# Performance work log

Hardware: AMD Instinct MI355X
Metric: run time of the kernel (lower is better)

Reference implementation:

```python
import jax, jax.numpy as jnp
import numpy as np

B, N, D, H = 2048, 100, 512, 8
TANH_C = 10.0


def setup_inputs() -> dict:
    key = jax.random.key(0)
    ks = jax.random.split(key, 16)
    s = 1.0 / np.sqrt(D)
    inp = {
        "node_embeddings": jax.random.normal(ks[0], (B, N, D), jnp.float32),
        "graph_embedding": jax.random.normal(ks[1], (B, D), jnp.float32),
        "target_idx": jax.random.randint(ks[2], (B,), 0, N, jnp.int32),
        "mask": jax.random.randint(ks[3], (B, N), 0, 2, jnp.int32),
    }
    for i, name in enumerate(["W_target", "W_global", "W_K1", "W_K2", "W_Q", "W_V",
                              "Wq_mha", "Wk_mha", "Wv_mha", "Wo_mha"]):
        inp[name] = jax.random.normal(ks[4 + i], (D, D), jnp.float32) * s
    return inp


def reference(node_embeddings, graph_embedding, target_idx, mask,
              W_target, W_global, W_K1, W_K2, W_Q, W_V,
              Wq_mha, Wk_mha, Wv_mha, Wo_mha):
    # one pointer-network decode step (Decoder loop body)
    b, n, d = node_embeddings.shape
    dh = d // H
    scale_h = 1.0 / (dh ** 0.5)

    # target_embeddings = node_embeddings[arange(B), env.target_stack]
    tgt = jnp.take_along_axis(node_embeddings, target_idx[:, None, None].astype(jnp.int32), axis=1)[:, 0, :]  # [B,D]

    # context = W_target(tgt) + W_global(graph)   (nn.Linear: x @ W.T)
    context = (tgt @ W_target.T + graph_embedding @ W_global.T)[:, None, :]  # [B,1,D]
    node_keys = node_embeddings @ W_K1.T   # [B,N,D]
    node_vals = node_embeddings @ W_V.T    # [B,N,D]

    # MultiHeadAttention([context, keys, values]) with internal per-head projections
    q = (context @ Wq_mha.T).reshape(b, 1, H, dh)
    k = (node_keys @ Wk_mha.T).reshape(b, n, H, dh)
    v = (node_vals @ Wv_mha.T).reshape(b, n, H, dh)
    scores = jnp.einsum("bqhd,bnhd->bhqn", q, k) * scale_h   # [B,H,1,N]
    attn = jax.nn.softmax(scores, axis=-1)
    mha = jnp.einsum("bhqn,bnhd->bqhd", attn, v).reshape(b, 1, d) @ Wo_mha.T  # [B,1,D]

    query = mha @ W_Q.T                    # [B,1,D]
    key2 = node_embeddings @ W_K2.T        # [B,N,D]

    # logits = (query @ key2^T) / sqrt(D), tanh-clipped, masked
    logits = jnp.einsum("bqd,bnd->bqn", query, key2)[:, 0, :] / (d ** 0.5)  # [B,N]
    logits = TANH_C * jnp.tanh(logits)
    logits = logits - mask.astype(logits.dtype) * 1e9
    log_p = jax.nn.log_softmax(logits, axis=1)  # [B,N]
    return log_p
```

## Files before the change

### kernel.cpp

```cpp
#include <hip/hip_runtime.h>

#define DD 512
#define NNODE 100
#define NH 8

typedef __attribute__((ext_vector_type(4))) float f32x4;
typedef __attribute__((ext_vector_type(8))) short s16x8;

__device__ __forceinline__ unsigned short f2bf(float x) {
  union { float f; unsigned int u; } v; v.f = x;
  unsigned int r = v.u + 0x7fffu + ((v.u >> 16) & 1u);
  return (unsigned short)(r >> 16);
}
__device__ __forceinline__ float bf2f(unsigned short u) {
  union { unsigned int u; float f; } v; v.u = ((unsigned int)u) << 16;
  return v.f;
}

__device__ __forceinline__ void gemm_accum(
    f32x4 acc[2][2], const float* __restrict__ A, const float* __restrict__ B,
    const int* __restrict__ gidx, int gmul, int K, int lda, int ldb,
    int transB, int m0, int n0,
    unsigned short (*As)[40], unsigned short (*Bs)[40])
{
  const int t = threadIdx.x;
  const int wid = t >> 6, lane = t & 63;
  const int wr = wid >> 1, wc = wid & 1;
  const int r16 = lane & 15, kg = (lane >> 4) * 8;
  const int tr = t >> 3, kq = t & 7;
  const int bn = t & 63, bk = t >> 6;

  for (int k0 = 0; k0 < K; k0 += 32) {
#pragma unroll
    for (int rp = 0; rp < 2; ++rp) {
      const int row = tr + rp * 32;
      const int gi = m0 + row;
      long ab = (long)gi * lda;
      if (gidx) ab += (long)gidx[gi] * gmul;
      const float4 av = *(const float4*)(A + ab + k0 + kq * 4);
      unsigned int p0 = (unsigned)f2bf(av.x) | ((unsigned)f2bf(av.y) << 16);
      unsigned int p1 = (unsigned)f2bf(av.z) | ((unsigned)f2bf(av.w) << 16);
      *(uint2*)(&As[row][kq * 4]) = make_uint2(p0, p1);
    }
    if (transB) {
#pragma unroll
      for (int rp = 0; rp < 2; ++rp) {
        const int row = tr + rp * 32;
        const float4 bv = *(const float4*)(B + (long)(n0 + row) * ldb + k0 + kq * 4);
        unsigned int p0 = (unsigned)f2bf(bv.x) | ((unsigned)f2bf(bv.y) << 16);
        unsigned int p1 = (unsigned)f2bf(bv.z) | ((unsigned)f2bf(bv.w) << 16);
        *(uint2*)(&Bs[row][kq * 4]) = make_uint2(p0, p1);
      }
    } else {
#pragma unroll
      for (int pp = 0; pp < 8; ++pp) {
        const int k = bk + pp * 4;
        Bs[bn][k] = f2bf(B[(long)(k0 + k) * ldb + n0 + bn]);
      }
    }
    __syncthreads();
    s16x8 a0 = *(const s16x8*)(&As[wr * 32 + r16][kg]);
    s16x8 a1 = *(const s16x8*)(&As[wr * 32 + 16 + r16][kg]);
    s16x8 b0 = *(const s16x8*)(&Bs[wc * 32 + r16][kg]);
    s16x8 b1 = *(const s16x8*)(&Bs[wc * 32 + 16 + r16][kg]);
    acc[0][0] = __builtin_amdgcn_mfma_f32_16x16x32_bf16(a0, b0, acc[0][0], 0, 0, 0);
    acc[0][1] = __builtin_amdgcn_mfma_f32_16x16x32_bf16(a0, b1, acc[0][1], 0, 0, 0);
    acc[1][0] = __builtin_amdgcn_mfma_f32_16x16x32_bf16(a1, b0, acc[1][0], 0, 0, 0);
    acc[1][1] = __builtin_amdgcn_mfma_f32_16x16x32_bf16(a1, b1, acc[1][1], 0, 0, 0);
    __syncthreads();
  }
}

__device__ __forceinline__ void gemm_epilogue(
    f32x4 acc[2][2], void* Cv, int ldc, float alpha, float beta, int obf16,
    int m0, int n0)
{
  const int t = threadIdx.x;
  const int wid = t >> 6, lane = t & 63;
  const int wr = wid >> 1, wc = wid & 1;
  const int r16 = lane & 15;
#pragma unroll
  for (int si = 0; si < 2; ++si)
#pragma unroll
    for (int sj = 0; sj < 2; ++sj)
#pragma unroll
      for (int r = 0; r < 4; ++r) {
        const int row = m0 + wr * 32 + si * 16 + (lane >> 4) * 4 + r;
        const int col = n0 + wc * 32 + sj * 16 + r16;
        const long ci = (long)row * ldc + col;
        float v = alpha * acc[si][sj][r];
        if (obf16) {
          ((unsigned short*)Cv)[ci] = f2bf(v);
        } else {
          float* C = (float*)Cv;
          if (beta != 0.f) v = fmaf(beta, C[ci], v);
          C[ci] = v;
        }
      }
}

__global__ __launch_bounds__(256) void gemm_mfma(
    const float* __restrict__ A, const float* __restrict__ B, void* Cv,
    int K, int lda, int ldb, int ldc,
    long aoffz, long boffz, long coffz,
    int transB, float alpha, float beta, int obf16)
{
  __shared__ unsigned short As[64][40];
  __shared__ unsigned short Bs[64][40];
  A += (long)blockIdx.z * aoffz;
  B += (long)blockIdx.z * boffz;
  f32x4 acc[2][2] = {};
  gemm_accum(acc, A, B, nullptr, 0, K, lda, ldb, transB,
             blockIdx.y * 64, blockIdx.x * 64, As, Bs);
  void* Cz = obf16 ? (void*)((unsigned short*)Cv + (long)blockIdx.z * coffz)
                   : (void*)((float*)Cv + (long)blockIdx.z * coffz);
  gemm_epilogue(acc, Cz, ldc, alpha, beta, obf16, blockIdx.y * 64, blockIdx.x * 64);
}

struct Fold5Args {
  const float* A[5]; const float* B[5]; float* C[5]; float al[5];
};

__global__ __launch_bounds__(256) void fold5_kernel(Fold5Args fa) {
  __shared__ unsigned short As[64][40];
  __shared__ unsigned short Bs[64][40];
  const int z = blockIdx.z;
  f32x4 acc[2][2] = {};
  gemm_accum(acc, fa.A[z], fa.B[z], nullptr, 0, 512, 512, 512, 0,
             blockIdx.y * 64, blockIdx.x * 64, As, Bs);
  gemm_epilogue(acc, fa.C[z], 512, fa.al[z], 0.f, 0, blockIdx.y * 64, blockIdx.x * 64);
}

__global__ __launch_bounds__(256) void qbuf_kernel(
    const float* __restrict__ node, const float* __restrict__ graph,
    const int* __restrict__ tidx, const float* __restrict__ A1,
    const float* __restrict__ A2, float* __restrict__ C)
{
  __shared__ unsigned short As[64][40];
  __shared__ unsigned short Bs[64][40];
  f32x4 acc[2][2] = {};
  gemm_accum(acc, node, A1, tidx, DD, DD, NNODE * DD, DD, 1,
             blockIdx.y * 64, blockIdx.x * 64, As, Bs);
  __syncthreads();
  gemm_accum(acc, graph, A2, nullptr, 0, DD, DD, DD, 1,
             blockIdx.y * 64, blockIdx.x * 64, As, Bs);
  gemm_epilogue(acc, C, DD, 1.f, 0.f, 0, blockIdx.y * 64, blockIdx.x * 64);
}

__global__ __launch_bounds__(256) void attn_fused(
    const float* __restrict__ node, const unsigned short* __restrict__ qk16,
    unsigned short* __restrict__ nb16, float* __restrict__ ctx)
{
  const int b = blockIdx.x;
  const int t = threadIdx.x;
  const int lane = t & 63;
  const int wid = t >> 6;
  const int r16 = lane & 15;
  const int rg = lane >> 4;

  __shared__ unsigned short nf[2][16 * 512];
  __shared__ unsigned short qf[16 * 288];
  __shared__ float Pl[4][16][8];
  __shared__ float rfl[4][8];

  {
    const unsigned short* qb = qk16 + (long)b * (NH * DD);
    for (int slot = t; slot < 512; slot += 256) {
      const int s = slot >> 5;
      const int idx = slot & 31;
      const int h = idx >> 2, g = idx & 3;
      *(s16x8*)(&qf[s * 288 + idx * 8 + (idx >> 3) * 8]) =
          *(const s16x8*)(qb + h * DD + s * 32 + g * 8);
    }
  }

  const int r0 = t >> 7;
  const int c4 = (t * 4) & 511;
  const int slotbase = ((c4 >> 3) * 16) + r0;
  const int j_c = c4 & 7;
  const int d0 = t * 2;
  const int cslot0 = (d0 >> 3) * 16;
  const int cxor = (d0 >> 3) & 7;
  const int cj = d0 & 7;
  const int qidx = (r16 & 7) * 4 + rg;
  const int qfb = qidx * 8 + (qidx >> 3) * 8;

  const float* nbase = node + (long)b * (NNODE * DD);
  float4 rs[8];
  {
    const int lim = NNODE * DD;
#pragma unroll
    for (int i = 0; i < 8; ++i) {
      const int e = 4 * t + 1024 * i;
      rs[i] = (e < lim) ? *(const float4*)(nbase + e) : make_float4(0.f, 0.f, 0.f, 0.f);
    }
  }

  float m = -3.0e38f, l = 0.f;
  float2 c2[NH];
#pragma unroll
  for (int h = 0; h < NH; ++h) { c2[h].x = 0.f; c2[h].y = 0.f; }
  ushort4 h4s[8];

  for (int c = 0; c < 7; ++c) {
    const int c0 = c * 16;
    const int cur = c & 1;
#pragma unroll
    for (int i = 0; i < 8; ++i) {
      ushort4 h4;
      h4.x = f2bf(rs[i].x); h4.y = f2bf(rs[i].y);
      h4.z = f2bf(rs[i].z); h4.w = f2bf(rs[i].w);
      h4s[i] = h4;
      const int slot = slotbase + 2 * i;
      const int phys = slot ^ ((slot >> 4) & 7);
      *(ushort4*)(&nf[cur][phys * 8 + j_c]) = h4;
    }
    __syncthreads();
    if (c < 6) {
      const int nc0 = c0 + 16;
      const int lim = (NNODE - nc0) * DD;
#pragma unroll
      for (int i = 0; i < 8; ++i) {
        const int e = 4 * t + 1024 * i;
        rs[i] = (e < lim) ? *(const float4*)(nbase + (long)nc0 * DD + e)
                          : make_float4(0.f, 0.f, 0.f, 0.f);
      }
    }
#pragma unroll
    for (int i = 0; i < 8; ++i) {
      const int row = r0 + 2 * i;
      if (c0 + row < NNODE)
        *(ushort4*)(nb16 + ((long)b * NNODE + c0 + row) * DD + c4) = h4s[i];
    }

    f32x4 acc = {0.f, 0.f, 0.f, 0.f};
#pragma unroll
    for (int s = 0; s < 16; ++s) {
      const int slr = (s * 4 + rg) * 16 + r16;
      const s16x8 av = *(const s16x8*)(&nf[cur][(slr ^ ((s * 4 + rg) & 7)) * 8]);
      s16x8 bv = {0, 0, 0, 0, 0, 0, 0, 0};
      if (r16 < NH) bv = *(const s16x8*)(&qf[s * 288 + qfb]);
      acc = __builtin_amdgcn_mfma_f32_16x16x32_bf16(av, bv, acc, 0, 0, 0);
    }
#pragma unroll
    for (int r = 0; r < 4; ++r)
      if (c0 + rg * 4 + r >= NNODE) acc[r] = -3.0e38f;

    float cm = fmaxf(fmaxf(acc[0], acc[1]), fmaxf(acc[2], acc[3]));
    cm = fmaxf(cm, __shfl_xor(cm, 16));
    cm = fmaxf(cm, __shfl_xor(cm, 32));
    const float mn = fmaxf(m, cm);
    const float rf = __expf(m - mn);
    float p[4], ps = 0.f;
#pragma unroll
    for (int r = 0; r < 4; ++r) { p[r] = __expf(acc[r] - mn); ps += p[r]; }
    ps += __shfl_xor(ps, 16);
    ps += __shfl_xor(ps, 32);
    l = l * rf + ps;
    m = mn;
    if (r16 < NH) {
#pragma unroll
      for (int r = 0; r < 4; ++r) Pl[wid][rg * 4 + r][r16] = p[r];
      if (rg == 0) rfl[wid][r16] = rf;
    }
    asm volatile("s_waitcnt lgkmcnt(0)" ::: "memory");

    {
      const f32x4 rf0 = *(const f32x4*)(&rfl[wid][0]);
      const f32x4 rf1 = *(const f32x4*)(&rfl[wid][4]);
#pragma unroll
      for (int h = 0; h < 4; ++h) { c2[h].x *= rf0[h]; c2[h].y *= rf0[h]; }
#pragma unroll
      for (int h = 0; h < 4; ++h) { c2[4 + h].x *= rf1[h]; c2[4 + h].y *= rf1[h]; }
#pragma unroll
      for (int n = 0; n < 16; ++n) {
        const int cphys = (cslot0 + n) ^ cxor;
        const unsigned int nv = *(const unsigned int*)(&nf[cur][cphys * 8 + cj]);
        const float x0 = bf2f((unsigned short)(nv & 0xffffu));
        const float x1 = bf2f((unsigned short)(nv >> 16));
        const f32x4 p0 = *(const f32x4*)(&Pl[wid][n][0]);
        const f32x4 p1 = *(const f32x4*)(&Pl[wid][n][4]);
#pragma unroll
        for (int h = 0; h < 4; ++h) {
          c2[h].x = fmaf(p0[h], x0, c2[h].x);
          c2[h].y = fmaf(p0[h], x1, c2[h].y);
          c2[4 + h].x = fmaf(p1[h], x0, c2[4 + h].x);
          c2[4 + h].y = fmaf(p1[h], x1, c2[4 + h].y);
        }
      }
    }
  }

  if (r16 < NH && rg == 0) rfl[wid][r16] = 1.f / l;
  asm volatile("s_waitcnt lgkmcnt(0)" ::: "memory");
  {
    const f32x4 i0 = *(const f32x4*)(&rfl[wid][0]);
    const f32x4 i1 = *(const f32x4*)(&rfl[wid][4]);
    float* cb = ctx + (long)b * (NH * DD) + d0;
#pragma unroll
    for (int h = 0; h < 4; ++h) {
      cb[h * DD] = c2[h].x * i0[h];
      cb[h * DD + 1] = c2[h].y * i0[h];
      cb[(4 + h) * DD] = c2[4 + h].x * i1[h];
      cb[(4 + h) * DD + 1] = c2[4 + h].y * i1[h];
    }
  }
}

__global__ __launch_bounds__(256) void logits_kernel(
    const unsigned short* __restrict__ nb16, const unsigned short* __restrict__ qk216,
    const int* __restrict__ mask, float* __restrict__ out)
{
  const int b = blockIdx.x;
  const int t = threadIdx.x;
  const int wid = t >> 6, lane = t & 63;
  const int r16 = lane & 15, rg = lane >> 4;
  __shared__ float sl[112];
  const unsigned short* qb = qk216 + (long)b * DD + rg * 8;

  for (int ti = wid; ti < 7; ti += 4) {
    const int arow = min(ti * 16 + r16, NNODE - 1);
    const unsigned short* ap = nb16 + ((long)b * NNODE + arow) * DD + rg * 8;
    f32x4 acc = {0.f, 0.f, 0.f, 0.f};
#pragma unroll
    for (int s = 0; s < 16; ++s) {
      const s16x8 av = *(const s16x8*)(ap + s * 32);
      const s16x8 bv = *(const s16x8*)(qb + s * 32);
      acc = __builtin_amdgcn_mfma_f32_16x16x32_bf16(av, bv, acc, 0, 0, 0);
    }
    if (r16 == 0) {
#pragma unroll
      for (int r = 0; r < 4; ++r) {
        const int n = ti * 16 + rg * 4 + r;
        if (n < 112) sl[n] = acc[r];
      }
    }
  }
  __syncthreads();
  if (t < 64) {
    float v0 = -3.0e38f, v1 = -3.0e38f;
    if (lane < NNODE)
      v0 = 10.f * tanhf(sl[lane]) - (float)mask[b * NNODE + lane] * 1e9f;
    if (lane + 64 < NNODE)
      v1 = 10.f * tanhf(sl[lane + 64]) - (float)mask[b * NNODE + lane + 64] * 1e9f;
    float mx = fmaxf(v0, v1);
#pragma unroll
    for (int off = 1; off < 64; off <<= 1) mx = fmaxf(mx, __shfl_xor(mx, off));
    float e = 0.f;
    if (lane < NNODE) e += __expf(v0 - mx);
    if (lane + 64 < NNODE) e += __expf(v1 - mx);
#pragma unroll
    for (int off = 1; off < 64; off <<= 1) e += __shfl_xor(e, off);
    const float lse = mx + __logf(e);
    float* ob = out + (long)b * NNODE;
    if (lane < NNODE) ob[lane] = v0 - lse;
    if (lane + 64 < NNODE) ob[lane + 64] = v1 - lse;
  }
}

extern "C" void kernel_launch(void* const* d_in, const int* in_sizes, int n_in,
                              void* d_out, int out_size, void* d_ws, size_t ws_size,
                              hipStream_t stream) {
  const float* node     = (const float*)d_in[0];
  const float* graph    = (const float*)d_in[1];
  const int*   tidx     = (const int*)d_in[2];
  const int*   mask     = (const int*)d_in[3];
  const float* W_target = (const float*)d_in[4];
  const float* W_global = (const float*)d_in[5];
  const float* W_K1     = (const float*)d_in[6];
  const float* W_K2     = (const float*)d_in[7];
  const float* W_Q      = (const float*)d_in[8];
  const float* W_V      = (const float*)d_in[9];
  const float* Wq_mha   = (const float*)d_in[10];
  const float* Wk_mha   = (const float*)d_in[11];
  const float* Wv_mha   = (const float*)d_in[12];
  const float* Wo_mha   = (const float*)d_in[13];
  float* out = (float*)d_out;

  float* base = (float*)d_ws;
  unsigned short* nb16 = (unsigned short*)base;
  long off = 2048L * NNODE * DD / 2;
  float* A1 = base + off;        off += 262144;
  float* A2 = base + off;        off += 262144;
  float* Wkc = base + off;       off += 262144;
  float* Wvc = base + off;       off += 262144;
  float* Woq = base + off;       off += 262144;
  float* qbuf = base + off;      off += 2048L * 512;
  unsigned short* qk16 = (unsigned short*)(base + off);  off += 2048L * 4096 / 2;
  float* ctxb = base + off;      off += 2048L * 4096;
  float* preo = base + off;      off += 2048L * 512;
  float* query = base + off;     off += 2048L * 512;
  unsigned short* qk216 = (unsigned short*)(base + off); off += 2048L * 512 / 2;

  dim3 blk(256);
  const float SH = 0.125f;
  const float SD = 0.044194173824f;

  Fold5Args fa;
  fa.A[0] = Wq_mha;  fa.B[0] = W_target; fa.C[0] = A1;  fa.al[0] = 1.f;
  fa.A[1] = Wq_mha;  fa.B[1] = W_global; fa.C[1] = A2;  fa.al[1] = 1.f;
  fa.A[2] = Wk_mha;  fa.B[2] = W_K1;     fa.C[2] = Wkc; fa.al[2] = SH;
  fa.A[3] = Wv_mha;  fa.B[3] = W_V;      fa.C[3] = Wvc; fa.al[3] = 1.f;
  fa.A[4] = W_Q;     fa.B[4] = Wo_mha;   fa.C[4] = Woq; fa.al[4] = 1.f;
  fold5_kernel<<<dim3(8, 8, 5), blk, 0, stream>>>(fa);
  qbuf_kernel<<<dim3(8, 32), blk, 0, stream>>>(node, graph, tidx, A1, A2, qbuf);
  gemm_mfma<<<dim3(8, 32, 8), blk, 0, stream>>>(qbuf, Wkc, qk16,
      64, 512, 512, 4096, 64, 32768, 512, 0, 1.f, 0.f, 1);
  attn_fused<<<dim3(2048), dim3(256), 0, stream>>>(node, qk16, nb16, ctxb);
  gemm_mfma<<<dim3(1, 32, 8), blk, 0, stream>>>(ctxb, Wvc, preo,
      512, 4096, 512, 512, 512, 32768, 64, 1, 1.f, 0.f, 0);
  gemm_mfma<<<dim3(8, 32, 1), blk, 0, stream>>>(preo, Woq, query,
      512, 512, 512, 512, 0, 0, 0, 1, 1.f, 0.f, 0);
  gemm_mfma<<<dim3(8, 32, 1), blk, 0, stream>>>(query, W_K2, qk216,
      512, 512, 512, 512, 0, 0, 0, 0, SD, 0.f, 1);
  logits_kernel<<<dim3(2048), blk, 0, stream>>>(nb16, qk216, mask, out);

  (void)in_sizes; (void)n_in; (void)out_size; (void)ws_size;
}
```

Measured before the change: 338.8 us.

## Fold Wo·W_Q·W_K2 weights, register-prefetch GEMM tiles, single-buffer attention smem

Precomputes M1 = Wo_mha^T·(W_Q^T·W_K2) in the weight-fold stage, merged into the qbuf kernel launch. This removes one per-batch 2048x512x512 GEMM and one launch from the activation path. The GEMM core now issues the next k-tile's global loads into registers before the MFMAs, overlapping load latency with compute. The attention kernel drops the double-buffered node tile to a single buffer plus an extra barrier, halving that LDS use to allow more occupancy at the cost of less overlap.

Result: faster. 300.7 us (-11.3%).

```diff
diff --git a/kernel.cpp b/kernel.cpp
--- a/kernel.cpp
+++ b/kernel.cpp
@@ -17,48 +17,91 @@
   return v.f;
 }
 
-__device__ __forceinline__ void gemm_accum(
+struct StageRegs { float4 a4[2]; float as[8]; float4 b4[2]; float bs[8]; };
+
+__device__ __forceinline__ void stage_issue(
+    StageRegs& r, const float* __restrict__ A, const float* __restrict__ B,
+    const int* __restrict__ gidx, int gmul, int k0, int lda, int ldb,
+    int transA, int transB, int m0, int n0)
+{
+  const int t = threadIdx.x;
+  const int tr = t >> 3, kq = t & 7;
+  const int bn = t & 63, bk = t >> 6;
+  if (!transA) {
+#pragma unroll
+    for (int rp = 0; rp < 2; ++rp) {
+      const int gi = m0 + tr + rp * 32;
+      long ab = (long)gi * lda;
+      if (gidx) ab += (long)gidx[gi] * gmul;
+      r.a4[rp] = *(const float4*)(A + ab + k0 + kq * 4);
+    }
+  } else {
+#pragma unroll
+    for (int pp = 0; pp < 8; ++pp)
+      r.as[pp] = A[(long)(k0 + bk + pp * 4) * lda + m0 + bn];
+  }
+  if (transB) {
+#pragma unroll
+    for (int rp = 0; rp < 2; ++rp)
+      r.b4[rp] = *(const float4*)(B + (long)(n0 + tr + rp * 32) * ldb + k0 + kq * 4);
+  } else {
+#pragma unroll
+    for (int pp = 0; pp < 8; ++pp)
+      r.bs[pp] = B[(long)(k0 + bk + pp * 4) * ldb + n0 + bn];
+  }
+}
+
+__device__ __forceinline__ void stage_commit(
+    const StageRegs& r, int transA, int transB,
+    unsigned short (*As)[40], unsigned short (*Bs)[40])
+{
+  const int t = threadIdx.x;
+  const int tr = t >> 3, kq = t & 7;
+  const int bn = t & 63, bk = t >> 6;
+  if (!transA) {
+#pragma unroll
+    for (int rp = 0; rp < 2; ++rp) {
+      const float4 av = r.a4[rp];
+      unsigned int p0 = (unsigned)f2bf(av.x) | ((unsigned)f2bf(av.y) << 16);
+      unsigned int p1 = (unsigned)f2bf(av.z) | ((unsigned)f2bf(av.w) << 16);
+      *(uint2*)(&As[tr + rp * 32][kq * 4]) = make_uint2(p0, p1);
+    }
+  } else {
+#pragma unroll
+    for (int pp = 0; pp < 8; ++pp) As[bn][bk + pp * 4] = f2bf(r.as[pp]);
+  }
+  if (transB) {
+#pragma unroll
+    for (int rp = 0; rp < 2; ++rp) {
+      const float4 bv = r.b4[rp];
+      unsigned int p0 = (unsigned)f2bf(bv.x) | ((unsigned)f2bf(bv.y) << 16);
+      unsigned int p1 = (unsigned)f2bf(bv.z) | ((unsigned)f2bf(bv.w) << 16);
+      *(uint2*)(&Bs[tr + rp * 32][kq * 4]) = make_uint2(p0, p1);
+    }
+  } else {
+#pragma unroll
+    for (int pp = 0; pp < 8; ++pp) Bs[bn][bk + pp * 4] = f2bf(r.bs[pp]);
+  }
+}
+
+__device__ __forceinline__ void gemm_core(
     f32x4 acc[2][2], const float* __restrict__ A, const float* __restrict__ B,
     const int* __restrict__ gidx, int gmul, int K, int lda, int ldb,
-    int transB, int m0, int n0,
+    int transA, int transB, int m0, int n0,
     unsigned short (*As)[40], unsigned short (*Bs)[40])
 {
   const int t = threadIdx.x;
   const int wid = t >> 6, lane = t & 63;
   const int wr = wid >> 1, wc = wid & 1;
   const int r16 = lane & 15, kg = (lane >> 4) * 8;
-  const int tr = t >> 3, kq = t & 7;
-  const int bn = t & 63, bk = t >> 6;
-
+  StageRegs r;
+  stage_issue(r, A, B, gidx, gmul, 0, lda, ldb, transA, transB, m0, n0);
   for (int k0 = 0; k0 < K; k0 += 32) {
-#pragma unroll
-    for (int rp = 0; rp < 2; ++rp) {
-      const int row = tr + rp * 32;
-      const int gi = m0 + row;
-      long ab = (long)gi * lda;
-      if (gidx) ab += (long)gidx[gi] * gmul;
-      const float4 av = *(const float4*)(A + ab + k0 + kq * 4);
-      unsigned int p0 = (unsigned)f2bf(av.x) | ((unsigned)f2bf(av.y) << 16);
-      unsigned int p1 = (unsigned)f2bf(av.z) | ((unsigned)f2bf(av.w) << 16);
-      *(uint2*)(&As[row][kq * 4]) = make_uint2(p0, p1);
-    }
-    if (transB) {
-#pragma unroll
-      for (int rp = 0; rp < 2; ++rp) {
-        const int row = tr + rp * 32;
-        const float4 bv = *(const float4*)(B + (long)(n0 + row) * ldb + k0 + kq * 4);
-        unsigned int p0 = (unsigned)f2bf(bv.x) | ((unsigned)f2bf(bv.y) << 16);
-        unsigned int p1 = (unsigned)f2bf(bv.z) | ((unsigned)f2bf(bv.w) << 16);
-        *(uint2*)(&Bs[row][kq * 4]) = make_uint2(p0, p1);
-      }
-    } else {
-#pragma unroll
-      for (int pp = 0; pp < 8; ++pp) {
-        const int k = bk + pp * 4;
-        Bs[bn][k] = f2bf(B[(long)(k0 + k) * ldb + n0 + bn]);
-      }
-    }
     __syncthreads();
+    stage_commit(r, transA, transB, As, Bs);
+    __syncthreads();
+    if (k0 + 32 < K)
+      stage_issue(r, A, B, gidx, gmul, k0 + 32, lda, ldb, transA, transB, m0, n0);
     s16x8 a0 = *(const s16x8*)(&As[wr * 32 + r16][kg]);
     s16x8 a1 = *(const s16x8*)(&As[wr * 32 + 16 + r16][kg]);
     s16x8 b0 = *(const s16x8*)(&Bs[wc * 32 + r16][kg]);
@@ -67,7 +110,6 @@
     acc[0][1] = __builtin_amdgcn_mfma_f32_16x16x32_bf16(a0, b1, acc[0][1], 0, 0, 0);
     acc[1][0] = __builtin_amdgcn_mfma_f32_16x16x32_bf16(a1, b0, acc[1][0], 0, 0, 0);
     acc[1][1] = __builtin_amdgcn_mfma_f32_16x16x32_bf16(a1, b1, acc[1][1], 0, 0, 0);
-    __syncthreads();
   }
 }
 
@@ -103,22 +145,22 @@
     const float* __restrict__ A, const float* __restrict__ B, void* Cv,
     int K, int lda, int ldb, int ldc,
     long aoffz, long boffz, long coffz,
-    int transB, float alpha, float beta, int obf16)
+    int transA, int transB, float alpha, float beta, int obf16)
 {
   __shared__ unsigned short As[64][40];
   __shared__ unsigned short Bs[64][40];
   A += (long)blockIdx.z * aoffz;
   B += (long)blockIdx.z * boffz;
   f32x4 acc[2][2] = {};
-  gemm_accum(acc, A, B, nullptr, 0, K, lda, ldb, transB,
-             blockIdx.y * 64, blockIdx.x * 64, As, Bs);
+  gemm_core(acc, A, B, nullptr, 0, K, lda, ldb, transA, transB,
+            blockIdx.y * 64, blockIdx.x * 64, As, Bs);
   void* Cz = obf16 ? (void*)((unsigned short*)Cv + (long)blockIdx.z * coffz)
                    : (void*)((float*)Cv + (long)blockIdx.z * coffz);
   gemm_epilogue(acc, Cz, ldc, alpha, beta, obf16, blockIdx.y * 64, blockIdx.x * 64);
 }
 
 struct Fold5Args {
-  const float* A[5]; const float* B[5]; float* C[5]; float al[5];
+  const float* A[5]; const float* B[5]; float* C[5]; float al[5]; int ta[5];
 };
 
 __global__ __launch_bounds__(256) void fold5_kernel(Fold5Args fa) {
@@ -126,25 +168,32 @@
   __shared__ unsigned short Bs[64][40];
   const int z = blockIdx.z;
   f32x4 acc[2][2] = {};
-  gemm_accum(acc, fa.A[z], fa.B[z], nullptr, 0, 512, 512, 512, 0,
-             blockIdx.y * 64, blockIdx.x * 64, As, Bs);
+  gemm_core(acc, fa.A[z], fa.B[z], nullptr, 0, 512, 512, 512, fa.ta[z], 0,
+            blockIdx.y * 64, blockIdx.x * 64, As, Bs);
   gemm_epilogue(acc, fa.C[z], 512, fa.al[z], 0.f, 0, blockIdx.y * 64, blockIdx.x * 64);
 }
 
-__global__ __launch_bounds__(256) void qbuf_kernel(
+__global__ __launch_bounds__(256) void qbufM1_kernel(
     const float* __restrict__ node, const float* __restrict__ graph,
     const int* __restrict__ tidx, const float* __restrict__ A1,
-    const float* __restrict__ A2, float* __restrict__ C)
+    const float* __restrict__ A2, float* __restrict__ qbuf,
+    const float* __restrict__ Wo, const float* __restrict__ T1,
+    float* __restrict__ M1)
 {
   __shared__ unsigned short As[64][40];
   __shared__ unsigned short Bs[64][40];
   f32x4 acc[2][2] = {};
-  gemm_accum(acc, node, A1, tidx, DD, DD, NNODE * DD, DD, 1,
-             blockIdx.y * 64, blockIdx.x * 64, As, Bs);
-  __syncthreads();
-  gemm_accum(acc, graph, A2, nullptr, 0, DD, DD, DD, 1,
-             blockIdx.y * 64, blockIdx.x * 64, As, Bs);
-  gemm_epilogue(acc, C, DD, 1.f, 0.f, 0, blockIdx.y * 64, blockIdx.x * 64);
+  const int n0 = blockIdx.x * 64;
+  if (blockIdx.y < 32) {
+    const int m0 = blockIdx.y * 64;
+    gemm_core(acc, node, A1, tidx, DD, DD, NNODE * DD, DD, 0, 1, m0, n0, As, Bs);
+    gemm_core(acc, graph, A2, nullptr, 0, DD, DD, DD, 0, 1, m0, n0, As, Bs);
+    gemm_epilogue(acc, qbuf, DD, 1.f, 0.f, 0, m0, n0);
+  } else {
+    const int m0 = (blockIdx.y - 32) * 64;
+    gemm_core(acc, Wo, T1, nullptr, 0, 512, 512, 512, 1, 0, m0, n0, As, Bs);
+    gemm_epilogue(acc, M1, 512, 1.f, 0.f, 0, m0, n0);
+  }
 }
 
 __global__ __launch_bounds__(256) void attn_fused(
@@ -158,7 +207,7 @@
   const int r16 = lane & 15;
   const int rg = lane >> 4;
 
-  __shared__ unsigned short nf[2][16 * 512];
+  __shared__ unsigned short nf[16 * 512];
   __shared__ unsigned short qf[16 * 288];
   __shared__ float Pl[4][16][8];
   __shared__ float rfl[4][8];
@@ -204,7 +253,6 @@
 
   for (int c = 0; c < 7; ++c) {
     const int c0 = c * 16;
-    const int cur = c & 1;
 #pragma unroll
     for (int i = 0; i < 8; ++i) {
       ushort4 h4;
@@ -213,7 +261,7 @@
       h4s[i] = h4;
       const int slot = slotbase + 2 * i;
       const int phys = slot ^ ((slot >> 4) & 7);
-      *(ushort4*)(&nf[cur][phys * 8 + j_c]) = h4;
+      *(ushort4*)(&nf[phys * 8 + j_c]) = h4;
     }
     __syncthreads();
     if (c < 6) {
@@ -237,7 +285,7 @@
 #pragma unroll
     for (int s = 0; s < 16; ++s) {
       const int slr = (s * 4 + rg) * 16 + r16;
-      const s16x8 av = *(const s16x8*)(&nf[cur][(slr ^ ((s * 4 + rg) & 7)) * 8]);
+      const s16x8 av = *(const s16x8*)(&nf[(slr ^ ((s * 4 + rg) & 7)) * 8]);
       s16x8 bv = {0, 0, 0, 0, 0, 0, 0, 0};
       if (r16 < NH) bv = *(const s16x8*)(&qf[s * 288 + qfb]);
       acc = __builtin_amdgcn_mfma_f32_16x16x32_bf16(av, bv, acc, 0, 0, 0);
@@ -275,7 +323,7 @@
 #pragma unroll
       for (int n = 0; n < 16; ++n) {
         const int cphys = (cslot0 + n) ^ cxor;
-        const unsigned int nv = *(const unsigned int*)(&nf[cur][cphys * 8 + cj]);
+        const unsigned int nv = *(const unsigned int*)(&nf[cphys * 8 + cj]);
         const float x0 = bf2f((unsigned short)(nv & 0xffffu));
         const float x1 = bf2f((unsigned short)(nv >> 16));
         const f32x4 p0 = *(const f32x4*)(&Pl[wid][n][0]);
@@ -289,6 +337,7 @@
         }
       }
     }
+    __syncthreads();
   }
 
   if (r16 < NH && rg == 0) rfl[wid][r16] = 1.f / l;
@@ -384,12 +433,12 @@
   float* A2 = base + off;        off += 262144;
   float* Wkc = base + off;       off += 262144;
   float* Wvc = base + off;       off += 262144;
-  float* Woq = base + off;       off += 262144;
+  float* T1 = base + off;        off += 262144;
+  float* M1 = base + off;        off += 262144;
   float* qbuf = base + off;      off += 2048L * 512;
   unsigned short* qk16 = (unsigned short*)(base + off);  off += 2048L * 4096 / 2;
   float* ctxb = base + off;      off += 2048L * 4096;
   float* preo = base + off;      off += 2048L * 512;
-  float* query = base + off;     off += 2048L * 512;
   unsigned short* qk216 = (unsigned short*)(base + off); off += 2048L * 512 / 2;
 
   dim3 blk(256);
@@ -397,22 +446,21 @@
   const float SD = 0.044194173824f;
 
   Fold5Args fa;
-  fa.A[0] = Wq_mha;  fa.B[0] = W_target; fa.C[0] = A1;  fa.al[0] = 1.f;
-  fa.A[1] = Wq_mha;  fa.B[1] = W_global; fa.C[1] = A2;  fa.al[1] = 1.f;
-  fa.A[2] = Wk_mha;  fa.B[2] = W_K1;     fa.C[2] = Wkc; fa.al[2] = SH;
-  fa.A[3] = Wv_mha;  fa.B[3] = W_V;      fa.C[3] = Wvc; fa.al[3] = 1.f;
-  fa.A[4] = W_Q;     fa.B[4] = Wo_mha;   fa.C[4] = Woq; fa.al[4] = 1.f;
+  fa.A[0] = Wq_mha;  fa.B[0] = W_target; fa.C[0] = A1;  fa.al[0] = 1.f; fa.ta[0] = 0;
+  fa.A[1] = Wq_mha;  fa.B[1] = W_global; fa.C[1] = A2;  fa.al[1] = 1.f; fa.ta[1] = 0;
+  fa.A[2] = Wk_mha;  fa.B[2] = W_K1;     fa.C[2] = Wkc; fa.al[2] = SH;  fa.ta[2] = 0;
+  fa.A[3] = Wv_mha;  fa.B[3] = W_V;      fa.C[3] = Wvc; fa.al[3] = 1.f; fa.ta[3] = 0;
+  fa.A[4] = W_Q;     fa.B[4] = W_K2;     fa.C[4] = T1;  fa.al[4] = 1.f; fa.ta[4] = 1;
   fold5_kernel<<<dim3(8, 8, 5), blk, 0, stream>>>(fa);
-  qbuf_kernel<<<dim3(8, 32), blk, 0, stream>>>(node, graph, tidx, A1, A2, qbuf);
+  qbufM1_kernel<<<dim3(8, 40), blk, 0, stream>>>(node, graph, tidx, A1, A2, qbuf,
+                                                 Wo_mha, T1, M1);
   gemm_mfma<<<dim3(8, 32, 8), blk, 0, stream>>>(qbuf, Wkc, qk16,
-      64, 512, 512, 4096, 64, 32768, 512, 0, 1.f, 0.f, 1);
-  attn_fused<<<dim3(2048), dim3(256), 0, stream>>>(node, qk16, nb16, ctxb);
+      64, 512, 512, 4096, 64, 32768, 512, 0, 0, 1.f, 0.f, 1);
+  attn_fused<<<dim3(2048), blk, 0, stream>>>(node, qk16, nb16, ctxb);
   gemm_mfma<<<dim3(1, 32, 8), blk, 0, stream>>>(ctxb, Wvc, preo,
-      512, 4096, 512, 512, 512, 32768, 64, 1, 1.f, 0.f, 0);
-  gemm_mfma<<<dim3(8, 32, 1), blk, 0, stream>>>(preo, Woq, query,
-      512, 512, 512, 512, 0, 0, 0, 1, 1.f, 0.f, 0);
-  gemm_mfma<<<dim3(8, 32, 1), blk, 0, stream>>>(query, W_K2, qk216,
-      512, 512, 512, 512, 0, 0, 0, 0, SD, 0.f, 1);
+      512, 4096, 512, 512, 512, 32768, 64, 0, 1, 1.f, 0.f, 0);
+  gemm_mfma<<<dim3(8, 32, 1), blk, 0, stream>>>(preo, M1, qk216,
+      512, 512, 512, 512, 0, 0, 0, 0, 0, SD, 0.f, 1);
   logits_kernel<<<dim3(2048), blk, 0, stream>>>(nb16, qk216, mask, out);
 
   (void)in_sizes; (void)n_in; (void)out_size; (void)ws_size;
```
